# Kernel optimization log

Hardware: AMD Instinct MI355X
Metric: run time of the kernel (lower is better)

## Reference

```python
import math
import jax, jax.numpy as jnp
import numpy as np

DIM = 2048
HID = 4 * DIM
SEQ = 2048
BATCH = 2
EPS = 1e-5


def _layernorm(x, g, b):
    mu = jnp.mean(x, axis=-1, keepdims=True)
    var = jnp.var(x, axis=-1, keepdims=True)
    return (x - mu) * jax.lax.rsqrt(var + EPS) * g + b


def setup_inputs() -> dict:
    key = jax.random.key(0)
    ks = jax.random.split(key, 12)
    s = 1.0 / math.sqrt(DIM)
    x = jax.random.normal(ks[0], (BATCH, SEQ, DIM), dtype=jnp.float32)
    # additive causal mask: 0 on/below diagonal, -1e9 above
    mask = jnp.where(jnp.tril(jnp.ones((SEQ, SEQ), dtype=bool)), 0.0, -1e9).astype(jnp.float32)
    freqs_cis = jax.random.normal(ks[1], (SEQ, 64), dtype=jnp.float32)  # unused by forward
    return {
        "x": x,
        "mask": mask,
        "start_pos": 0,
        "freqs_cis": freqs_cis,
        "wq": jax.random.normal(ks[2], (DIM, DIM), dtype=jnp.float32) * s,
        "bq": jnp.zeros((DIM,), dtype=jnp.float32),
        "wk": jax.random.normal(ks[3], (DIM, DIM), dtype=jnp.float32) * s,
        "bk": jnp.zeros((DIM,), dtype=jnp.float32),
        "wv": jax.random.normal(ks[4], (DIM, DIM), dtype=jnp.float32) * s,
        "bv": jnp.zeros((DIM,), dtype=jnp.float32),
        "g_ln1": jnp.ones((DIM,), dtype=jnp.float32),
        "b_ln1": jnp.zeros((DIM,), dtype=jnp.float32),
        "g_ln2": jnp.ones((DIM,), dtype=jnp.float32),
        "b_ln2": jnp.zeros((DIM,), dtype=jnp.float32),
        "w1": jax.random.normal(ks[5], (DIM, HID), dtype=jnp.float32) * s,
        "b1": jnp.zeros((HID,), dtype=jnp.float32),
        "w2": jax.random.normal(ks[6], (HID, DIM), dtype=jnp.float32) * (1.0 / math.sqrt(HID)),
        "b2": jnp.zeros((DIM,), dtype=jnp.float32),
    }


def reference(x, mask, start_pos, freqs_cis, wq, bq, wk, bk, wv, bv,
              g_ln1, b_ln1, g_ln2, b_ln2, w1, b1, w2, b2):
    # pre-norm attention (no head split; scale by sqrt(full dim); dropout=eval identity)
    h = _layernorm(x, g_ln1, b_ln1)
    q = h @ wq + bq
    k = h @ wk + bk
    v = h @ wv + bv
    scores = jnp.einsum('bqd,bkd->bqk', q, k) / math.sqrt(DIM) + mask
    attn = jax.nn.softmax(scores, axis=-1)
    attn_out = jnp.einsum('bqk,bkd->bqd', attn, v)
    h2 = _layernorm(x + attn_out, g_ln2, b_ln2)
    ffn = jax.nn.gelu(h2 @ w1 + b1, approximate=False) @ w2 + b2
    # NOTE: original code adds FFN output to the ORIGINAL x (attn residual dropped here)
    return x + ffn
```

## Files before the change

### kernel.cpp

```cpp
#include <hip/hip_runtime.h>
#include <math.h>

#define DIM_ 2048
#define HID_ 8192
#define SEQ_ 2048
#define BATCH_ 2
#define TOK_ (BATCH_*SEQ_)

typedef __attribute__((ext_vector_type(4))) float f32x4;
typedef __attribute__((ext_vector_type(8))) __bf16 bf16x8;
typedef __attribute__((ext_vector_type(4))) unsigned int u32x4;
typedef __attribute__((ext_vector_type(4))) short s16x4;
typedef __attribute__((address_space(3))) short* lds_sp;

__device__ __forceinline__ short f2bf(float f) {
  union { float f; unsigned u; } v; v.f = f;
  unsigned r = v.u + 0x7FFFu + ((v.u >> 16) & 1u);
  return (short)(r >> 16);
}

__device__ __forceinline__ f32x4 mfma16(u32x4 a, u32x4 b, f32x4 c) {
  return __builtin_amdgcn_mfma_f32_16x16x32_bf16(
      __builtin_bit_cast(bf16x8, a), __builtin_bit_cast(bf16x8, b), c, 0, 0, 0);
}

#define DSR(dst, addr) asm volatile("ds_read_b128 %0, %1" : "=v"(dst) : "v"(addr))

#define RD_A(mlo, slot) do { \
  const unsigned ab_ = aBase + (unsigned)(slot)*16384u + (mlo)*2048u; \
  DSR(af[0][0], ab_ + offk0);         DSR(af[0][1], ab_ + offk1); \
  DSR(af[1][0], ab_ + 2048u + offk0); DSR(af[1][1], ab_ + 2048u + offk1); \
} while(0)

#define RD_B(slot) do { \
  const unsigned bb_ = bBase + (unsigned)(slot)*32768u; \
  DSR(bfr[0][0], bb_ + offk0);         DSR(bfr[0][1], bb_ + offk1); \
  DSR(bfr[1][0], bb_ + 2048u + offk0); DSR(bfr[1][1], bb_ + 2048u + offk1); \
  DSR(bfr[2][0], bb_ + 4096u + offk0); DSR(bfr[2][1], bb_ + 4096u + offk1); \
  DSR(bfr[3][0], bb_ + 6144u + offk0); DSR(bfr[3][1], bb_ + 6144u + offk1); \
} while(0)

#define MM(mlo) do { \
  _Pragma("unroll") \
  for (int n_ = 0; n_ < 4; ++n_) { \
    acc[(mlo)][n_]   = mfma16(af[0][0], bfr[n_][0], acc[(mlo)][n_]); \
    acc[(mlo)][n_]   = mfma16(af[0][1], bfr[n_][1], acc[(mlo)][n_]); \
    acc[(mlo)+1][n_] = mfma16(af[1][0], bfr[n_][0], acc[(mlo)+1][n_]); \
    acc[(mlo)+1][n_] = mfma16(af[1][1], bfr[n_][1], acc[(mlo)+1][n_]); \
  } \
} while(0)

#define BARv()  __builtin_amdgcn_s_barrier()
#define LGKM0() do { asm volatile("s_waitcnt lgkmcnt(0)" ::: "memory"); \
                     __builtin_amdgcn_sched_barrier(0); } while(0)
#define LGKM8() asm volatile("s_waitcnt lgkmcnt(8)" ::: "memory")
#define VM6()   asm volatile("s_waitcnt vmcnt(6)" ::: "memory")

template<int EPI>
__global__ __launch_bounds__(512, 2)
void gemm8p(const short* __restrict__ A, const short* __restrict__ B,
            void* __restrict__ Cv, const float* __restrict__ bias,
            const float* __restrict__ aux,
            int M, int N, int K, int lda, int ldb, int ldc,
            long long sA, long long sB, long long sC)
{
  __shared__ __align__(16) short As[3*128*64];
  __shared__ __align__(16) short Bs[3*256*64];
  const int lane = threadIdx.x & 63;
  const int wave = threadIdx.x >> 6;
  const int wr = wave >> 2, wc = wave & 3;
  const int nwg  = gridDim.x * gridDim.y;
  const int orig = blockIdx.y * gridDim.x + blockIdx.x;
  const int wgid = (orig & 7) * (nwg >> 3) + (orig >> 3);
  const int tn = (wgid % gridDim.x) * 256;
  const int tm = (wgid / gridDim.x) * 128;
  const int z  = blockIdx.z;
  A += (long long)z * sA;
  B += (long long)z * sB;

  const int NT = K >> 6;

  const int lr    = lane >> 3;
  const int lrow  = wave * 8 + lr;
  const int lslot = ((lane & 7) ^ lr) << 3;
  const short* pA = A + (long long)(tm + lrow) * lda + lslot;
  const short* pB = B + (long long)(tn + lrow) * ldb + lslot;
  const long long lda64 = 64LL * lda;
  const long long ldb64 = 64LL * ldb;

  auto stageA = [&](int t, int slot) {
    const long long ko = (long long)t << 6;
    const int db = slot * 8192 + wave * 512;
    __builtin_amdgcn_global_load_lds(
        (const __attribute__((address_space(1))) void*)(pA + ko),
        (__attribute__((address_space(3))) void*)(As + db), 16, 0, 0);
    __builtin_amdgcn_global_load_lds(
        (const __attribute__((address_space(1))) void*)(pA + lda64 + ko),
        (__attribute__((address_space(3))) void*)(As + db + 4096), 16, 0, 0);
  };
  auto stageB = [&](int t, int slot) {
    const long long ko = (long long)t << 6;
    const int db = slot * 16384 + wave * 512;
    __builtin_amdgcn_global_load_lds(
        (const __attribute__((address_space(1))) void*)(pB + ko),
        (__attribute__((address_space(3))) void*)(Bs + db), 16, 0, 0);
    __builtin_amdgcn_global_load_lds(
        (const __attribute__((address_space(1))) void*)(pB + ldb64 + ko),
        (__attribute__((address_space(3))) void*)(Bs + db + 4096), 16, 0, 0);
    __builtin_amdgcn_global_load_lds(
        (const __attribute__((address_space(1))) void*)(pB + 2*ldb64 + ko),
        (__attribute__((address_space(3))) void*)(Bs + db + 8192), 16, 0, 0);
    __builtin_amdgcn_global_load_lds(
        (const __attribute__((address_space(1))) void*)(pB + 3*ldb64 + ko),
        (__attribute__((address_space(3))) void*)(Bs + db + 12288), 16, 0, 0);
  };

  const unsigned asB = (unsigned)(unsigned long long)(lds_sp)As;
  const unsigned bsB = (unsigned)(unsigned long long)(lds_sp)Bs;
  const int l15 = lane & 15, l4 = lane >> 4;
  const unsigned offk0 = (unsigned)(( l4      ^ (lane & 7)) << 4);
  const unsigned offk1 = (unsigned)(((l4 + 4) ^ (lane & 7)) << 4);
  const unsigned aBase = asB + (unsigned)((wr * 64 + l15) * 128);
  const unsigned bBase = bsB + (unsigned)((wc * 64 + l15) * 128);

  f32x4 acc[4][4] = {};
  u32x4 af[2][2], bfr[4][2];

  stageB(0, 0); stageA(0, 0);
  stageB(1 < NT ? 1 : 0, 1); stageA(1 < NT ? 1 : 0, 1);
  VM6();
  BARv();

  int rd = 0;
  #pragma unroll 1
  for (int t = 0; t < NT; ++t) {
    const int st = rd + 2 >= 3 ? rd - 1 : rd + 2;
    const int tc = t + 2 < NT ? t + 2 : NT - 1;
    RD_A(0, rd); RD_B(rd);
    stageB(tc, st);
    LGKM8();
    BARv(); LGKM0();
    __builtin_amdgcn_s_setprio(1); MM(0); __builtin_amdgcn_s_setprio(0);
    BARv();
    RD_A(2, rd);
    stageA(tc, st);
    VM6();
    BARv(); LGKM0();
    __builtin_amdgcn_s_setprio(1); MM(2); __builtin_amdgcn_s_setprio(0);
    BARv();
    rd = rd + 1 >= 3 ? 0 : rd + 1;
  }

  const int row0 = tm + wr * 64 + l4 * 4;
  const int col0 = tn + wc * 64 + l15;
  #pragma unroll
  for (int mi = 0; mi < 4; ++mi) {
    #pragma unroll
    for (int j = 0; j < 4; ++j) {
      const int row = row0 + mi * 16 + j;
      #pragma unroll
      for (int ni = 0; ni < 4; ++ni) {
        const int col = col0 + ni * 16;
        float v = acc[mi][ni][j];
        if (EPI == 1) {
          ((float*)Cv + (long long)z * sC)[(long long)row * ldc + col] = v;
        } else if (EPI == 0) {
          v += bias[col];
          ((short*)Cv + (long long)z * sC)[(long long)row * ldc + col] = f2bf(v);
        } else if (EPI == 2) {
          v += bias[col];
          v = 0.5f * v * (1.0f + erff(v * 0.70710678118654752f));
          ((short*)Cv + (long long)z * sC)[(long long)row * ldc + col] = f2bf(v);
        } else {
          v += bias[col] + aux[(long long)row * ldc + col];
          ((float*)Cv + (long long)z * sC)[(long long)row * ldc + col] = v;
        }
      }
    }
  }
}

__global__ __launch_bounds__(256)
void ln_kernel(const float* __restrict__ x, const float* __restrict__ res,
               const float* __restrict__ g, const float* __restrict__ b,
               short* __restrict__ out, int hasres)
{
  const int row = blockIdx.x;
  const int tid = threadIdx.x;
  const float4* X = (const float4*)x + (long long)row * 512;
  float4 v0 = X[tid], v1 = X[tid + 256];
  if (hasres) {
    const float4* R = (const float4*)res + (long long)row * 512;
    float4 r0 = R[tid], r1 = R[tid + 256];
    v0.x += r0.x; v0.y += r0.y; v0.z += r0.z; v0.w += r0.w;
    v1.x += r1.x; v1.y += r1.y; v1.z += r1.z; v1.w += r1.w;
  }
  float s1 = v0.x + v0.y + v0.z + v0.w + v1.x + v1.y + v1.z + v1.w;
  float s2 = v0.x*v0.x + v0.y*v0.y + v0.z*v0.z + v0.w*v0.w
           + v1.x*v1.x + v1.y*v1.y + v1.z*v1.z + v1.w*v1.w;
  #pragma unroll
  for (int o = 32; o > 0; o >>= 1) { s1 += __shfl_xor(s1, o); s2 += __shfl_xor(s2, o); }
  __shared__ float red[8];
  if ((tid & 63) == 0) { red[tid >> 6] = s1; red[4 + (tid >> 6)] = s2; }
  __syncthreads();
  s1 = red[0] + red[1] + red[2] + red[3];
  s2 = red[4] + red[5] + red[6] + red[7];
  const float mean = s1 * (1.0f / 2048.0f);
  const float var  = s2 * (1.0f / 2048.0f) - mean * mean;
  const float rstd = rsqrtf(var + 1e-5f);
  const float4* G  = (const float4*)g;
  const float4* Bb = (const float4*)b;
  float4 g0 = G[tid], g1 = G[tid + 256], b0 = Bb[tid], b1 = Bb[tid + 256];
  s16x4 o0, o1;
  o0[0] = f2bf((v0.x - mean) * rstd * g0.x + b0.x);
  o0[1] = f2bf((v0.y - mean) * rstd * g0.y + b0.y);
  o0[2] = f2bf((v0.z - mean) * rstd * g0.z + b0.z);
  o0[3] = f2bf((v0.w - mean) * rstd * g0.w + b0.w);
  o1[0] = f2bf((v1.x - mean) * rstd * g1.x + b1.x);
  o1[1] = f2bf((v1.y - mean) * rstd * g1.y + b1.y);
  o1[2] = f2bf((v1.z - mean) * rstd * g1.z + b1.z);
  o1[3] = f2bf((v1.w - mean) * rstd * g1.w + b1.w);
  *(s16x4*)&out[(long long)row * 2048 + tid * 4]        = o0;
  *(s16x4*)&out[(long long)row * 2048 + 1024 + tid * 4] = o1;
}

__global__ __launch_bounds__(256)
void softmax_kernel(const float* __restrict__ scores, const float* __restrict__ mask,
                    short* __restrict__ probs)
{
  const long long row = blockIdx.x;
  const int q  = blockIdx.x & (SEQ_ - 1);
  const int tid = threadIdx.x;
  const float scale = 0.022097086912079608f;
  const float4* S  = (const float4*)scores + row * 512;
  const float4* Mk = (const float4*)mask + (long long)q * 512;
  float4 v0 = S[tid], v1 = S[tid + 256];
  float4 m0 = Mk[tid], m1 = Mk[tid + 256];
  float a[8] = { v0.x*scale + m0.x, v0.y*scale + m0.y, v0.z*scale + m0.z, v0.w*scale + m0.w,
                 v1.x*scale + m1.x, v1.y*scale + m1.y, v1.z*scale + m1.z, v1.w*scale + m1.w };
  float mx = a[0];
  #pragma unroll
  for (int i = 1; i < 8; ++i) mx = fmaxf(mx, a[i]);
  #pragma unroll
  for (int o = 32; o > 0; o >>= 1) mx = fmaxf(mx, __shfl_xor(mx, o));
  __shared__ float red[8];
  if ((tid & 63) == 0) red[tid >> 6] = mx;
  __syncthreads();
  mx = fmaxf(fmaxf(red[0], red[1]), fmaxf(red[2], red[3]));
  float e[8], sum = 0.f;
  #pragma unroll
  for (int i = 0; i < 8; ++i) { e[i] = __expf(a[i] - mx); sum += e[i]; }
  #pragma unroll
  for (int o = 32; o > 0; o >>= 1) sum += __shfl_xor(sum, o);
  if ((tid & 63) == 0) red[4 + (tid >> 6)] = sum;
  __syncthreads();
  sum = red[4] + red[5] + red[6] + red[7];
  const float inv = 1.0f / sum;
  s16x4 o0, o1;
  #pragma unroll
  for (int i = 0; i < 4; ++i) o0[i] = f2bf(e[i] * inv);
  #pragma unroll
  for (int i = 0; i < 4; ++i) o1[i] = f2bf(e[4 + i] * inv);
  probs += row * 2048;
  *(s16x4*)&probs[tid * 4]        = o0;
  *(s16x4*)&probs[1024 + tid * 4] = o1;
}

__global__ __launch_bounds__(256)
void cvt_transpose_kernel(const float* __restrict__ in, short* __restrict__ out,
                          int R, int C)
{
  __shared__ float t[32][33];
  const int tx = threadIdx.x & 31, ty = threadIdx.x >> 5;
  const int r0 = blockIdx.y << 5, c0 = blockIdx.x << 5;
  #pragma unroll
  for (int i = 0; i < 32; i += 8)
    t[ty + i][tx] = in[(long long)(r0 + ty + i) * C + c0 + tx];
  __syncthreads();
  #pragma unroll
  for (int i = 0; i < 32; i += 8)
    out[(long long)(c0 + ty + i) * R + r0 + tx] = f2bf(t[tx][ty + i]);
}

__global__ __launch_bounds__(256)
void transpose_bf16_kernel(const short* __restrict__ in, short* __restrict__ out,
                           int ldin, int ldout, long long sin_, long long sout_)
{
  __shared__ short t[32][33];
  in  += (long long)blockIdx.z * sin_;
  out += (long long)blockIdx.z * sout_;
  const int tx = threadIdx.x & 31, ty = threadIdx.x >> 5;
  const int r0 = blockIdx.y << 5, c0 = blockIdx.x << 5;
  #pragma unroll
  for (int i = 0; i < 32; i += 8)
    t[ty + i][tx] = in[(long long)(r0 + ty + i) * ldin + c0 + tx];
  __syncthreads();
  #pragma unroll
  for (int i = 0; i < 32; i += 8)
    out[(long long)(c0 + ty + i) * ldout + r0 + tx] = t[tx][ty + i];
}

__global__ __launch_bounds__(256)
void concat_bias_kernel(const float* a, const float* b, const float* c, float* o)
{
  const int i = blockIdx.x * 256 + threadIdx.x;
  o[i] = i < 2048 ? a[i] : (i < 4096 ? b[i - 2048] : c[i - 4096]);
}

extern "C" void kernel_launch(void* const* d_in, const int* in_sizes, int n_in,
                              void* d_out, int out_size, void* d_ws, size_t ws_size,
                              hipStream_t stream)
{
  const float* x    = (const float*)d_in[0];
  const float* mask = (const float*)d_in[1];
  const float* wq   = (const float*)d_in[4];
  const float* bq   = (const float*)d_in[5];
  const float* wk   = (const float*)d_in[6];
  const float* bk   = (const float*)d_in[7];
  const float* wv   = (const float*)d_in[8];
  const float* bv   = (const float*)d_in[9];
  const float* g1   = (const float*)d_in[10];
  const float* b1   = (const float*)d_in[11];
  const float* g2   = (const float*)d_in[12];
  const float* b2   = (const float*)d_in[13];
  const float* w1   = (const float*)d_in[14];
  const float* bw1  = (const float*)d_in[15];
  const float* w2   = (const float*)d_in[16];
  const float* bw2  = (const float*)d_in[17];
  float* out = (float*)d_out;

  char* p = (char*)d_ws;
  auto take = [&](size_t bytes) { char* r = p; p += (bytes + 255) & ~(size_t)255; return r; };
  short* wqkvT = (short*)take((size_t)3 * DIM_ * DIM_ * 2);
  short* w1T   = (short*)take((size_t)DIM_ * HID_ * 2);
  short* w2T   = (short*)take((size_t)HID_ * DIM_ * 2);
  short* h_bf  = (short*)take((size_t)TOK_ * DIM_ * 2);
  short* qkv   = (short*)take((size_t)TOK_ * 3 * DIM_ * 2);
  short* vT    = (short*)take((size_t)BATCH_ * DIM_ * SEQ_ * 2);
  float* scores= (float*)take((size_t)BATCH_ * SEQ_ * SEQ_ * 4);
  short* attn  = (short*)take((size_t)BATCH_ * SEQ_ * SEQ_ * 2);
  float* cbias = (float*)take((size_t)3 * DIM_ * 4);
  short* ffn1  = qkv;
  float* attno = scores;
  short* h2    = h_bf;

  const dim3 blk(256), gblk(512);
  cvt_transpose_kernel<<<dim3(DIM_/32, DIM_/32), blk, 0, stream>>>(wq, wqkvT, DIM_, DIM_);
  cvt_transpose_kernel<<<dim3(DIM_/32, DIM_/32), blk, 0, stream>>>(wk, wqkvT + (size_t)DIM_*DIM_, DIM_, DIM_);
  cvt_transpose_kernel<<<dim3(DIM_/32, DIM_/32), blk, 0, stream>>>(wv, wqkvT + (size_t)2*DIM_*DIM_, DIM_, DIM_);
  cvt_transpose_kernel<<<dim3(HID_/32, DIM_/32), blk, 0, stream>>>(w1, w1T, DIM_, HID_);
  cvt_transpose_kernel<<<dim3(DIM_/32, HID_/32), blk, 0, stream>>>(w2, w2T, HID_, DIM_);
  concat_bias_kernel<<<24, blk, 0, stream>>>(bq, bk, bv, cbias);
  ln_kernel<<<TOK_, blk, 0, stream>>>(x, nullptr, g1, b1, h_bf, 0);
  gemm8p<0><<<dim3(6144/256, TOK_/128, 1), gblk, 0, stream>>>(
      h_bf, wqkvT, qkv, cbias, nullptr, TOK_, 6144, DIM_, DIM_, DIM_, 6144, 0, 0, 0);
  gemm8p<1><<<dim3(SEQ_/256, SEQ_/128, BATCH_), gblk, 0, stream>>>(
      qkv, qkv + DIM_, scores, nullptr, nullptr, SEQ_, SEQ_, DIM_, 6144, 6144, SEQ_,
      (long long)SEQ_ * 6144, (long long)SEQ_ * 6144, (long long)SEQ_ * SEQ_);
  softmax_kernel<<<BATCH_ * SEQ_, blk, 0, stream>>>(scores, mask, attn);
  transpose_bf16_kernel<<<dim3(DIM_/32, SEQ_/32, BATCH_), blk, 0, stream>>>(
      qkv + 2*DIM_, vT, 6144, SEQ_, (long long)SEQ_ * 6144, (long long)DIM_ * SEQ_);
  gemm8p<1><<<dim3(DIM_/256, SEQ_/128, BATCH_), gblk, 0, stream>>>(
      attn, vT, attno, nullptr, nullptr, SEQ_, DIM_, SEQ_, SEQ_, SEQ_, DIM_,
      (long long)SEQ_ * SEQ_, (long long)DIM_ * SEQ_, (long long)SEQ_ * DIM_);
  ln_kernel<<<TOK_, blk, 0, stream>>>(x, attno, g2, b2, h2, 1);
  gemm8p<2><<<dim3(HID_/256, TOK_/128, 1), gblk, 0, stream>>>(
      h2, w1T, ffn1, bw1, nullptr, TOK_, HID_, DIM_, DIM_, DIM_, HID_, 0, 0, 0);
  gemm8p<3><<<dim3(DIM_/256, TOK_/128, 1), gblk, 0, stream>>>(
      ffn1, w2T, out, bw2, x, TOK_, DIM_, HID_, HID_, HID_, DIM_, 0, 0, 0);
}
```

Measured before the change: 641.6 us.

## Fuse score scaling and mask into QK GEMM, add high-occupancy FFN GEMM

The QK^T GEMM now applies the scale and additive mask in its epilogue and writes bf16 scores straight into the attention buffer. Softmax then runs in place on bf16 data, which removes the fp32 score round trip and the separate mask read. The FFN GEMMs move to a new kernel with K-step 32, smaller LDS and 4 blocks per CU, and all GEMMs get a grouped tile-ordering map. Weight conversion uses a 64x64 vectorised transpose. Storing pre-softmax scores in bf16 loses precision before the exponent.

Measured after the change: 626.2 us. 1.02x faster.

```diff
diff --git a/kernel.cpp b/kernel.cpp
--- a/kernel.cpp
+++ b/kernel.cpp
@@ -11,6 +11,7 @@
 typedef __attribute__((ext_vector_type(8))) __bf16 bf16x8;
 typedef __attribute__((ext_vector_type(4))) unsigned int u32x4;
 typedef __attribute__((ext_vector_type(4))) short s16x4;
+typedef __attribute__((ext_vector_type(8))) short s16x8;
 typedef __attribute__((address_space(3))) short* lds_sp;
 
 __device__ __forceinline__ short f2bf(float f) {
@@ -18,6 +19,10 @@
   unsigned r = v.u + 0x7FFFu + ((v.u >> 16) & 1u);
   return (short)(r >> 16);
 }
+__device__ __forceinline__ float bf2f(short s) {
+  union { unsigned u; float f; } v; v.u = ((unsigned)(unsigned short)s) << 16;
+  return v.f;
+}
 
 __device__ __forceinline__ f32x4 mfma16(u32x4 a, u32x4 b, f32x4 c) {
   return __builtin_amdgcn_mfma_f32_16x16x32_bf16(
@@ -25,15 +30,55 @@
 }
 
 #define DSR(dst, addr) asm volatile("ds_read_b128 %0, %1" : "=v"(dst) : "v"(addr))
+#define BARv()  __builtin_amdgcn_s_barrier()
+#define LGKM0() do { asm volatile("s_waitcnt lgkmcnt(0)" ::: "memory"); \
+                     __builtin_amdgcn_sched_barrier(0); } while(0)
+#define LGKM8() asm volatile("s_waitcnt lgkmcnt(8)" ::: "memory")
+#define VM6()   asm volatile("s_waitcnt vmcnt(6)" ::: "memory")
+#define VM3()   asm volatile("s_waitcnt vmcnt(3)" ::: "memory")
+#define PRIO1() __builtin_amdgcn_s_setprio(1)
+#define PRIO0() __builtin_amdgcn_s_setprio(0)
+
+#define TILE_MAP(BM, BN) \
+  const int nwg  = gridDim.x * gridDim.y; \
+  const int orig = blockIdx.y * gridDim.x + blockIdx.x; \
+  const int wgid = (orig & 7) * (nwg >> 3) + (orig >> 3); \
+  const int gy4  = (int)gridDim.y << 2; \
+  const int rem  = wgid % gy4; \
+  const int tn   = ((wgid / gy4) * 4 + (rem & 3)) * (BN); \
+  const int tm   = (rem >> 2) * (BM);
+
+template<int EPI>
+__device__ __forceinline__ void epi_store(void* Cv, const float* bias, const float* aux,
+                                          int z, long long sC, int ldc, int N,
+                                          int row, int col, float v)
+{
+  if (EPI == 1) {
+    ((float*)Cv + (long long)z * sC)[(long long)row * ldc + col] = v;
+  } else if (EPI == 0) {
+    v += bias[col];
+    ((short*)Cv + (long long)z * sC)[(long long)row * ldc + col] = f2bf(v);
+  } else if (EPI == 2) {
+    v += bias[col];
+    v = 0.5f * v * (1.0f + erff(v * 0.70710678118654752f));
+    ((short*)Cv + (long long)z * sC)[(long long)row * ldc + col] = f2bf(v);
+  } else if (EPI == 3) {
+    v += bias[col] + aux[(long long)row * ldc + col];
+    ((float*)Cv + (long long)z * sC)[(long long)row * ldc + col] = v;
+  } else {
+    v = v * 0.022097086912079608f + aux[(long long)row * ldc + col];
+    ((short*)Cv + (long long)z * sC)[(long long)row * ldc + col] = f2bf(v);
+  }
+}
 
 #define RD_A(mlo, slot) do { \
-  const unsigned ab_ = aBase + (unsigned)(slot)*16384u + (mlo)*2048u; \
+  const unsigned ab_ = aBase8 + (unsigned)(slot)*16384u + (mlo)*2048u; \
   DSR(af[0][0], ab_ + offk0);         DSR(af[0][1], ab_ + offk1); \
   DSR(af[1][0], ab_ + 2048u + offk0); DSR(af[1][1], ab_ + 2048u + offk1); \
 } while(0)
 
 #define RD_B(slot) do { \
-  const unsigned bb_ = bBase + (unsigned)(slot)*32768u; \
+  const unsigned bb_ = bBase8 + (unsigned)(slot)*32768u; \
   DSR(bfr[0][0], bb_ + offk0);         DSR(bfr[0][1], bb_ + offk1); \
   DSR(bfr[1][0], bb_ + 2048u + offk0); DSR(bfr[1][1], bb_ + 2048u + offk1); \
   DSR(bfr[2][0], bb_ + 4096u + offk0); DSR(bfr[2][1], bb_ + 4096u + offk1); \
@@ -50,12 +95,6 @@
   } \
 } while(0)
 
-#define BARv()  __builtin_amdgcn_s_barrier()
-#define LGKM0() do { asm volatile("s_waitcnt lgkmcnt(0)" ::: "memory"); \
-                     __builtin_amdgcn_sched_barrier(0); } while(0)
-#define LGKM8() asm volatile("s_waitcnt lgkmcnt(8)" ::: "memory")
-#define VM6()   asm volatile("s_waitcnt vmcnt(6)" ::: "memory")
-
 template<int EPI>
 __global__ __launch_bounds__(512, 2)
 void gemm8p(const short* __restrict__ A, const short* __restrict__ B,
@@ -69,11 +108,7 @@
   const int lane = threadIdx.x & 63;
   const int wave = threadIdx.x >> 6;
   const int wr = wave >> 2, wc = wave & 3;
-  const int nwg  = gridDim.x * gridDim.y;
-  const int orig = blockIdx.y * gridDim.x + blockIdx.x;
-  const int wgid = (orig & 7) * (nwg >> 3) + (orig >> 3);
-  const int tn = (wgid % gridDim.x) * 256;
-  const int tm = (wgid / gridDim.x) * 128;
+  TILE_MAP(128, 256)
   const int z  = blockIdx.z;
   A += (long long)z * sA;
   B += (long long)z * sB;
@@ -120,8 +155,8 @@
   const int l15 = lane & 15, l4 = lane >> 4;
   const unsigned offk0 = (unsigned)(( l4      ^ (lane & 7)) << 4);
   const unsigned offk1 = (unsigned)(((l4 + 4) ^ (lane & 7)) << 4);
-  const unsigned aBase = asB + (unsigned)((wr * 64 + l15) * 128);
-  const unsigned bBase = bsB + (unsigned)((wc * 64 + l15) * 128);
+  const unsigned aBase8 = asB + (unsigned)((wr * 64 + l15) * 128);
+  const unsigned bBase8 = bsB + (unsigned)((wc * 64 + l15) * 128);
 
   f32x4 acc[4][4] = {};
   u32x4 af[2][2], bfr[4][2];
@@ -140,13 +175,13 @@
     stageB(tc, st);
     LGKM8();
     BARv(); LGKM0();
-    __builtin_amdgcn_s_setprio(1); MM(0); __builtin_amdgcn_s_setprio(0);
+    PRIO1(); MM(0); PRIO0();
     BARv();
     RD_A(2, rd);
     stageA(tc, st);
     VM6();
     BARv(); LGKM0();
-    __builtin_amdgcn_s_setprio(1); MM(2); __builtin_amdgcn_s_setprio(0);
+    PRIO1(); MM(2); PRIO0();
     BARv();
     rd = rd + 1 >= 3 ? 0 : rd + 1;
   }
@@ -154,30 +189,110 @@
   const int row0 = tm + wr * 64 + l4 * 4;
   const int col0 = tn + wc * 64 + l15;
   #pragma unroll
-  for (int mi = 0; mi < 4; ++mi) {
+  for (int mi = 0; mi < 4; ++mi)
     #pragma unroll
-    for (int j = 0; j < 4; ++j) {
-      const int row = row0 + mi * 16 + j;
+    for (int j = 0; j < 4; ++j)
       #pragma unroll
-      for (int ni = 0; ni < 4; ++ni) {
-        const int col = col0 + ni * 16;
-        float v = acc[mi][ni][j];
-        if (EPI == 1) {
-          ((float*)Cv + (long long)z * sC)[(long long)row * ldc + col] = v;
-        } else if (EPI == 0) {
-          v += bias[col];
-          ((short*)Cv + (long long)z * sC)[(long long)row * ldc + col] = f2bf(v);
-        } else if (EPI == 2) {
-          v += bias[col];
-          v = 0.5f * v * (1.0f + erff(v * 0.70710678118654752f));
-          ((short*)Cv + (long long)z * sC)[(long long)row * ldc + col] = f2bf(v);
-        } else {
-          v += bias[col] + aux[(long long)row * ldc + col];
-          ((float*)Cv + (long long)z * sC)[(long long)row * ldc + col] = v;
-        }
-      }
-    }
-  }
+      for (int ni = 0; ni < 4; ++ni)
+        epi_store<EPI>(Cv, bias, aux, z, sC, ldc, N,
+                       row0 + mi * 16 + j, col0 + ni * 16, acc[mi][ni][j]);
+}
+
+#define HRD(slot) do { \
+  const unsigned a_ = aBaseH + (unsigned)(slot)*8192u; \
+  const unsigned b_ = bBaseH + (unsigned)(slot)*16384u; \
+  DSR(af[0], a_ + offk);          DSR(af[1], a_ + 1024u + offk); \
+  DSR(af[2], a_ + 2048u + offk);  DSR(af[3], a_ + 3072u + offk); \
+  DSR(bf[0], b_ + offk);          DSR(bf[1], b_ + 1024u + offk); \
+  DSR(bf[2], b_ + 2048u + offk);  DSR(bf[3], b_ + 3072u + offk); \
+} while(0)
+
+#define HMM() do { \
+  _Pragma("unroll") \
+  for (int mi = 0; mi < 4; ++mi) \
+    _Pragma("unroll") \
+    for (int ni = 0; ni < 4; ++ni) \
+      acc[mi][ni] = mfma16(af[mi], bf[ni], acc[mi][ni]); \
+} while(0)
+
+template<int EPI>
+__global__ __launch_bounds__(512, 4)
+void gemm_hi(const short* __restrict__ A, const short* __restrict__ B,
+             void* __restrict__ Cv, const float* __restrict__ bias,
+             const float* __restrict__ aux,
+             int M, int N, int K, int lda, int ldb, int ldc,
+             long long sA, long long sB, long long sC)
+{
+  __shared__ __align__(16) short As[3*128*32];
+  __shared__ __align__(16) short Bs[3*256*32];
+  const int lane = threadIdx.x & 63;
+  const int wave = threadIdx.x >> 6;
+  const int wr = wave >> 2, wc = wave & 3;
+  TILE_MAP(128, 256)
+  const int z = blockIdx.z;
+  A += (long long)z * sA;
+  B += (long long)z * sB;
+
+  const int NT = K >> 5;
+
+  const int rr   = wave * 16 + (lane >> 2);
+  const int soff = (((lane & 3) ^ ((lane >> 2) & 3)) << 3);
+  const short* pA = A + (long long)(tm + rr) * lda + soff;
+  const short* pB = B + (long long)(tn + rr) * ldb + soff;
+  const long long ldb128 = 128LL * ldb;
+
+  auto stage = [&](int t, int slot) {
+    const long long ko = (long long)t << 5;
+    __builtin_amdgcn_global_load_lds(
+        (const __attribute__((address_space(1))) void*)(pA + ko),
+        (__attribute__((address_space(3))) void*)(As + slot * 4096 + wave * 512), 16, 0, 0);
+    __builtin_amdgcn_global_load_lds(
+        (const __attribute__((address_space(1))) void*)(pB + ko),
+        (__attribute__((address_space(3))) void*)(Bs + slot * 8192 + wave * 512), 16, 0, 0);
+    __builtin_amdgcn_global_load_lds(
+        (const __attribute__((address_space(1))) void*)(pB + ldb128 + ko),
+        (__attribute__((address_space(3))) void*)(Bs + slot * 8192 + 4096 + wave * 512), 16, 0, 0);
+  };
+
+  const unsigned asB = (unsigned)(unsigned long long)(lds_sp)As;
+  const unsigned bsB = (unsigned)(unsigned long long)(lds_sp)Bs;
+  const int l15 = lane & 15, l4 = lane >> 4;
+  const unsigned offk  = (unsigned)((l4 ^ (l15 & 3)) << 4);
+  const unsigned aBaseH = asB + (unsigned)(wr * 4096 + l15 * 64);
+  const unsigned bBaseH = bsB + (unsigned)(wc * 4096 + l15 * 64);
+
+  f32x4 acc[4][4] = {};
+  u32x4 af[4], bf[4];
+
+  stage(0, 0);
+  stage(1 < NT ? 1 : 0, 1);
+  VM3();
+  BARv();
+
+  int rd = 0;
+  #pragma unroll 1
+  for (int t = 0; t < NT; ++t) {
+    const int st = rd + 2 >= 3 ? rd - 1 : rd + 2;
+    const int tc = t + 2 < NT ? t + 2 : NT - 1;
+    HRD(rd);
+    stage(tc, st);
+    BARv(); LGKM0();
+    PRIO1(); HMM(); PRIO0();
+    VM3();
+    BARv();
+    rd = rd + 1 >= 3 ? 0 : rd + 1;
+  }
+
+  const int row0 = tm + wr * 64 + l4 * 4;
+  const int col0 = tn + wc * 64 + l15;
+  #pragma unroll
+  for (int mi = 0; mi < 4; ++mi)
+    #pragma unroll
+    for (int j = 0; j < 4; ++j)
+      #pragma unroll
+      for (int ni = 0; ni < 4; ++ni)
+        epi_store<EPI>(Cv, bias, aux, z, sC, ldc, N,
+                       row0 + mi * 16 + j, col0 + ni * 16, acc[mi][ni][j]);
 }
 
 __global__ __launch_bounds__(256)
@@ -225,19 +340,15 @@
 }
 
 __global__ __launch_bounds__(256)
-void softmax_kernel(const float* __restrict__ scores, const float* __restrict__ mask,
-                    short* __restrict__ probs)
+void softmax_bf16_kernel(short* __restrict__ probs)
 {
   const long long row = blockIdx.x;
-  const int q  = blockIdx.x & (SEQ_ - 1);
   const int tid = threadIdx.x;
-  const float scale = 0.022097086912079608f;
-  const float4* S  = (const float4*)scores + row * 512;
-  const float4* Mk = (const float4*)mask + (long long)q * 512;
-  float4 v0 = S[tid], v1 = S[tid + 256];
-  float4 m0 = Mk[tid], m1 = Mk[tid + 256];
-  float a[8] = { v0.x*scale + m0.x, v0.y*scale + m0.y, v0.z*scale + m0.z, v0.w*scale + m0.w,
-                 v1.x*scale + m1.x, v1.y*scale + m1.y, v1.z*scale + m1.z, v1.w*scale + m1.w };
+  short* P = probs + row * 2048 + tid * 8;
+  s16x8 in = *(const s16x8*)P;
+  float a[8];
+  #pragma unroll
+  for (int i = 0; i < 8; ++i) a[i] = bf2f(in[i]);
   float mx = a[0];
   #pragma unroll
   for (int i = 1; i < 8; ++i) mx = fmaxf(mx, a[i]);
@@ -256,30 +367,34 @@
   __syncthreads();
   sum = red[4] + red[5] + red[6] + red[7];
   const float inv = 1.0f / sum;
-  s16x4 o0, o1;
-  #pragma unroll
-  for (int i = 0; i < 4; ++i) o0[i] = f2bf(e[i] * inv);
-  #pragma unroll
-  for (int i = 0; i < 4; ++i) o1[i] = f2bf(e[4 + i] * inv);
-  probs += row * 2048;
-  *(s16x4*)&probs[tid * 4]        = o0;
-  *(s16x4*)&probs[1024 + tid * 4] = o1;
+  s16x8 o;
+  #pragma unroll
+  for (int i = 0; i < 8; ++i) o[i] = f2bf(e[i] * inv);
+  *(s16x8*)P = o;
 }
 
 __global__ __launch_bounds__(256)
-void cvt_transpose_kernel(const float* __restrict__ in, short* __restrict__ out,
-                          int R, int C)
-{
-  __shared__ float t[32][33];
-  const int tx = threadIdx.x & 31, ty = threadIdx.x >> 5;
-  const int r0 = blockIdx.y << 5, c0 = blockIdx.x << 5;
-  #pragma unroll
-  for (int i = 0; i < 32; i += 8)
-    t[ty + i][tx] = in[(long long)(r0 + ty + i) * C + c0 + tx];
+void cvt_transpose64(const float* __restrict__ in, short* __restrict__ out,
+                     int R, int C)
+{
+  __shared__ float t[64][69];
+  const int r0 = blockIdx.y << 6, c0 = blockIdx.x << 6;
+  const int tx = threadIdx.x & 15, ty = threadIdx.x >> 4;
+  #pragma unroll
+  for (int p = 0; p < 4; ++p) {
+    const int r = ty + p * 16;
+    float4 v = *(const float4*)&in[(long long)(r0 + r) * C + c0 + tx * 4];
+    t[r][tx*4+0] = v.x; t[r][tx*4+1] = v.y; t[r][tx*4+2] = v.z; t[r][tx*4+3] = v.w;
+  }
   __syncthreads();
   #pragma unroll
-  for (int i = 0; i < 32; i += 8)
-    out[(long long)(c0 + ty + i) * R + r0 + tx] = f2bf(t[tx][ty + i]);
+  for (int p = 0; p < 4; ++p) {
+    const int oc = ty + p * 16;
+    s16x4 o;
+    o[0] = f2bf(t[tx*4+0][oc]); o[1] = f2bf(t[tx*4+1][oc]);
+    o[2] = f2bf(t[tx*4+2][oc]); o[3] = f2bf(t[tx*4+3][oc]);
+    *(s16x4*)&out[(long long)(c0 + oc) * R + r0 + tx * 4] = o;
+  }
 }
 
 __global__ __launch_bounds__(256)
@@ -337,35 +452,34 @@
   short* h_bf  = (short*)take((size_t)TOK_ * DIM_ * 2);
   short* qkv   = (short*)take((size_t)TOK_ * 3 * DIM_ * 2);
   short* vT    = (short*)take((size_t)BATCH_ * DIM_ * SEQ_ * 2);
-  float* scores= (float*)take((size_t)BATCH_ * SEQ_ * SEQ_ * 4);
+  float* attno = (float*)take((size_t)TOK_ * DIM_ * 4);
   short* attn  = (short*)take((size_t)BATCH_ * SEQ_ * SEQ_ * 2);
   float* cbias = (float*)take((size_t)3 * DIM_ * 4);
   short* ffn1  = qkv;
-  float* attno = scores;
   short* h2    = h_bf;
 
   const dim3 blk(256), gblk(512);
-  cvt_transpose_kernel<<<dim3(DIM_/32, DIM_/32), blk, 0, stream>>>(wq, wqkvT, DIM_, DIM_);
-  cvt_transpose_kernel<<<dim3(DIM_/32, DIM_/32), blk, 0, stream>>>(wk, wqkvT + (size_t)DIM_*DIM_, DIM_, DIM_);
-  cvt_transpose_kernel<<<dim3(DIM_/32, DIM_/32), blk, 0, stream>>>(wv, wqkvT + (size_t)2*DIM_*DIM_, DIM_, DIM_);
-  cvt_transpose_kernel<<<dim3(HID_/32, DIM_/32), blk, 0, stream>>>(w1, w1T, DIM_, HID_);
-  cvt_transpose_kernel<<<dim3(DIM_/32, HID_/32), blk, 0, stream>>>(w2, w2T, HID_, DIM_);
+  cvt_transpose64<<<dim3(DIM_/64, DIM_/64), blk, 0, stream>>>(wq, wqkvT, DIM_, DIM_);
+  cvt_transpose64<<<dim3(DIM_/64, DIM_/64), blk, 0, stream>>>(wk, wqkvT + (size_t)DIM_*DIM_, DIM_, DIM_);
+  cvt_transpose64<<<dim3(DIM_/64, DIM_/64), blk, 0, stream>>>(wv, wqkvT + (size_t)2*DIM_*DIM_, DIM_, DIM_);
+  cvt_transpose64<<<dim3(HID_/64, DIM_/64), blk, 0, stream>>>(w1, w1T, DIM_, HID_);
+  cvt_transpose64<<<dim3(DIM_/64, HID_/64), blk, 0, stream>>>(w2, w2T, HID_, DIM_);
   concat_bias_kernel<<<24, blk, 0, stream>>>(bq, bk, bv, cbias);
   ln_kernel<<<TOK_, blk, 0, stream>>>(x, nullptr, g1, b1, h_bf, 0);
   gemm8p<0><<<dim3(6144/256, TOK_/128, 1), gblk, 0, stream>>>(
       h_bf, wqkvT, qkv, cbias, nullptr, TOK_, 6144, DIM_, DIM_, DIM_, 6144, 0, 0, 0);
-  gemm8p<1><<<dim3(SEQ_/256, SEQ_/128, BATCH_), gblk, 0, stream>>>(
-      qkv, qkv + DIM_, scores, nullptr, nullptr, SEQ_, SEQ_, DIM_, 6144, 6144, SEQ_,
+  gemm8p<4><<<dim3(SEQ_/256, SEQ_/128, BATCH_), gblk, 0, stream>>>(
+      qkv, qkv + DIM_, attn, nullptr, mask, SEQ_, SEQ_, DIM_, 6144, 6144, SEQ_,
       (long long)SEQ_ * 6144, (long long)SEQ_ * 6144, (long long)SEQ_ * SEQ_);
-  softmax_kernel<<<BATCH_ * SEQ_, blk, 0, stream>>>(scores, mask, attn);
+  softmax_bf16_kernel<<<BATCH_ * SEQ_, blk, 0, stream>>>(attn);
   transpose_bf16_kernel<<<dim3(DIM_/32, SEQ_/32, BATCH_), blk, 0, stream>>>(
       qkv + 2*DIM_, vT, 6144, SEQ_, (long long)SEQ_ * 6144, (long long)DIM_ * SEQ_);
   gemm8p<1><<<dim3(DIM_/256, SEQ_/128, BATCH_), gblk, 0, stream>>>(
       attn, vT, attno, nullptr, nullptr, SEQ_, DIM_, SEQ_, SEQ_, SEQ_, DIM_,
       (long long)SEQ_ * SEQ_, (long long)DIM_ * SEQ_, (long long)SEQ_ * DIM_);
   ln_kernel<<<TOK_, blk, 0, stream>>>(x, attno, g2, b2, h2, 1);
-  gemm8p<2><<<dim3(HID_/256, TOK_/128, 1), gblk, 0, stream>>>(
+  gemm_hi<2><<<dim3(HID_/256, TOK_/128, 1), gblk, 0, stream>>>(
       h2, w1T, ffn1, bw1, nullptr, TOK_, HID_, DIM_, DIM_, DIM_, HID_, 0, 0, 0);
-  gemm8p<3><<<dim3(DIM_/256, TOK_/128, 1), gblk, 0, stream>>>(
+  gemm_hi<3><<<dim3(DIM_/256, TOK_/128, 1), gblk, 0, stream>>>(
       ffn1, w2T, out, bw2, x, TOK_, DIM_, HID_, HID_, HID_, DIM_, 0, 0, 0);
 }
```
